# Kernel tuning notes

Measured on AMD Instinct MI355X. Metric: run time of the kernel, lower is better.

The kernel has to match this reference:

```python
import jax, jax.numpy as jnp
import numpy as np

B, L, D = 8, 4096, 768


def setup_inputs() -> dict:
    key = jax.random.key(0)
    k1, = jax.random.split(key, 1)
    x = jax.random.normal(k1, (B, L, D), dtype=jnp.float32)
    alpha = jnp.ones((L, 1), dtype=jnp.float32)  # nn.Parameter(torch.ones(l_dim, 1))
    return {"x": x, "alpha": alpha}


def reference(x, alpha):
    # Original: y = (x @ x^T).mean(-1, keepdim=True) / D
    # Algebraically identical (mean over j of sum_d x_i,d x_j,d = x_i . mean_j x_j):
    d = x.shape[-1]
    l = x.shape[1]
    mean_x = jnp.mean(x, axis=1)                       # [B, D]
    y = jnp.einsum('bld,bd->bl', x, mean_x)[..., None] / d  # [B, L, 1]
    # Original: y = (y @ y^T).mean(-1, keepdim=True) / L
    # (y y^T)_ij = y_i * y_j; mean over j = y_i * mean(y)
    y = y * jnp.mean(y, axis=1, keepdims=True) / l     # [B, L, 1]
    # y * x + alpha  (alpha broadcast over batch and D); dropout p=0 -> identity
    return alpha + y * x
```

## Files before the change

### kernel.cpp

```cpp
#include <hip/hip_runtime.h>

constexpr int Bn = 8;
constexpr int Ln = 4096;
constexpr int Dn = 768;
constexpr int NCH = 128;
constexpr int RPC = Ln / NCH;

typedef float f4 __attribute__((ext_vector_type(4)));

__global__ void k_colsum_part(const float* __restrict__ x, f4* __restrict__ part) {
    int b = blockIdx.x >> 7;
    int c = blockIdx.x & (NCH - 1);
    int t = threadIdx.x;
    const f4* xb = (const f4*)(x + ((size_t)b * Ln + (size_t)c * RPC) * Dn);
    f4 s = {0.f, 0.f, 0.f, 0.f};
    #pragma unroll 4
    for (int l = 0; l < RPC; ++l) {
        s += xb[(size_t)l * (Dn / 4) + t];
    }
    part[(size_t)blockIdx.x * (Dn / 4) + t] = s;
}

__global__ void k_scale(const float* __restrict__ part, float* __restrict__ m) {
    int b = blockIdx.x;
    int t = threadIdx.x;
    const float* pb = part + (size_t)b * NCH * Dn;
    float s0 = 0.f, s1 = 0.f, s2 = 0.f;
    for (int c = 0; c < NCH; ++c) {
        const float* row = pb + (size_t)c * Dn;
        s0 += row[t];
        s1 += row[t + 256];
        s2 += row[t + 512];
    }
    float ssq = s0 * s0 + s1 * s1 + s2 * s2;
    #pragma unroll
    for (int off = 1; off < 64; off <<= 1) ssq += __shfl_xor(ssq, off);
    __shared__ float wsum[4];
    int wave = t >> 6, lane = t & 63;
    if (lane == 0) wsum[wave] = ssq;
    __syncthreads();
    float ss = wsum[0] + wsum[1] + wsum[2] + wsum[3];

    const float f1 = 1.0f / ((float)Ln * (float)Dn);
    float scale = ss * f1 * f1 / ((float)Ln * (float)Ln);
    m[b * Dn + t]       = s0 * scale;
    m[b * Dn + t + 256] = s1 * scale;
    m[b * Dn + t + 512] = s2 * scale;
}

__global__ void k_fused(const float* __restrict__ x, const float* __restrict__ m,
                        const float* __restrict__ alpha, float* __restrict__ out) {
    int wave = threadIdx.x >> 6;
    int lane = threadIdx.x & 63;
    int row  = blockIdx.x * 4 + wave;
    int b    = row >> 12;
    int l    = row & (Ln - 1);

    const f4* xr = (const f4*)(x + (size_t)row * Dn);
    const f4* mr = (const f4*)(m + (size_t)b * Dn);

    f4 x0 = xr[lane], x1 = xr[lane + 64], x2 = xr[lane + 128];
    f4 m0 = mr[lane], m1 = mr[lane + 64], m2 = mr[lane + 128];

    f4 p = x0 * m0 + x1 * m1 + x2 * m2;
    float acc = p.x + p.y + p.z + p.w;
    #pragma unroll
    for (int off = 1; off < 64; off <<= 1) acc += __shfl_xor(acc, off);

    float a = alpha[l];
    f4* orow = (f4*)(out + (size_t)row * Dn);
    f4 o0 = a + acc * x0;
    f4 o1 = a + acc * x1;
    f4 o2 = a + acc * x2;
    __builtin_nontemporal_store(o0, &orow[lane]);
    __builtin_nontemporal_store(o1, &orow[lane + 64]);
    __builtin_nontemporal_store(o2, &orow[lane + 128]);
}

extern "C" void kernel_launch(void* const* d_in, const int* in_sizes, int n_in,
                              void* d_out, int out_size, void* d_ws, size_t ws_size,
                              hipStream_t stream) {
    const float* x     = (const float*)d_in[0];
    const float* alpha = (const float*)d_in[1];
    float* out = (float*)d_out;

    float* part = (float*)d_ws;
    float* m    = part + (size_t)Bn * NCH * Dn;

    k_colsum_part<<<Bn * NCH, 192, 0, stream>>>(x, (f4*)part);
    k_scale<<<Bn, 256, 0, stream>>>(part, m);
    k_fused<<<(Bn * Ln) / 4, 256, 0, stream>>>(x, m, alpha, out);
}
```

Measured before the change: 198.8 us.

## Fuse partial column-sum reduction into the main kernel, dropping the scale kernel

Removes the single-pass k_scale kernel. Each wave of the fused kernel now re-reduces all per-chunk partial sums for its batch and computes the global scale itself. The goal is to save a launch and the serial tail of an 8-block reduction kernel, at the cost of massive redundant reads of the partial buffer, which is mostly served from cache. The colsum loop unroll also rises from 4 to 8.

```diff
diff --git a/kernel.cpp b/kernel.cpp
--- a/kernel.cpp
+++ b/kernel.cpp
@@ -14,53 +14,42 @@
     int t = threadIdx.x;
     const f4* xb = (const f4*)(x + ((size_t)b * Ln + (size_t)c * RPC) * Dn);
     f4 s = {0.f, 0.f, 0.f, 0.f};
-    #pragma unroll 4
+    #pragma unroll 8
     for (int l = 0; l < RPC; ++l) {
         s += xb[(size_t)l * (Dn / 4) + t];
     }
     part[(size_t)blockIdx.x * (Dn / 4) + t] = s;
 }
 
-__global__ void k_scale(const float* __restrict__ part, float* __restrict__ m) {
-    int b = blockIdx.x;
-    int t = threadIdx.x;
-    const float* pb = part + (size_t)b * NCH * Dn;
-    float s0 = 0.f, s1 = 0.f, s2 = 0.f;
-    for (int c = 0; c < NCH; ++c) {
-        const float* row = pb + (size_t)c * Dn;
-        s0 += row[t];
-        s1 += row[t + 256];
-        s2 += row[t + 512];
-    }
-    float ssq = s0 * s0 + s1 * s1 + s2 * s2;
-    #pragma unroll
-    for (int off = 1; off < 64; off <<= 1) ssq += __shfl_xor(ssq, off);
-    __shared__ float wsum[4];
-    int wave = t >> 6, lane = t & 63;
-    if (lane == 0) wsum[wave] = ssq;
-    __syncthreads();
-    float ss = wsum[0] + wsum[1] + wsum[2] + wsum[3];
-
-    const float f1 = 1.0f / ((float)Ln * (float)Dn);
-    float scale = ss * f1 * f1 / ((float)Ln * (float)Ln);
-    m[b * Dn + t]       = s0 * scale;
-    m[b * Dn + t + 256] = s1 * scale;
-    m[b * Dn + t + 512] = s2 * scale;
-}
-
-__global__ void k_fused(const float* __restrict__ x, const float* __restrict__ m,
-                        const float* __restrict__ alpha, float* __restrict__ out) {
+__global__ void __launch_bounds__(256)
+k_fused(const float* __restrict__ x, const float* __restrict__ part,
+        const float* __restrict__ alpha, float* __restrict__ out) {
     int wave = threadIdx.x >> 6;
     int lane = threadIdx.x & 63;
     int row  = blockIdx.x * 4 + wave;
     int b    = row >> 12;
     int l    = row & (Ln - 1);
 
+    const f4* pb = (const f4*)part + (size_t)b * NCH * (Dn / 4);
+    f4 s0 = {0.f,0.f,0.f,0.f}, s1 = {0.f,0.f,0.f,0.f}, s2 = {0.f,0.f,0.f,0.f};
+    #pragma unroll 8
+    for (int c = 0; c < NCH; ++c) {
+        const f4* pr = pb + (size_t)c * (Dn / 4);
+        s0 += pr[lane];
+        s1 += pr[lane + 64];
+        s2 += pr[lane + 128];
+    }
+    f4 q = s0 * s0 + s1 * s1 + s2 * s2;
+    float ssq = q.x + q.y + q.z + q.w;
+    #pragma unroll
+    for (int off = 1; off < 64; off <<= 1) ssq += __shfl_xor(ssq, off);
+
+    const float f1 = 1.0f / ((float)Ln * (float)Dn);
+    float scale = ssq * f1 * f1 / ((float)Ln * (float)Ln);
+    f4 m0 = s0 * scale, m1 = s1 * scale, m2 = s2 * scale;
+
     const f4* xr = (const f4*)(x + (size_t)row * Dn);
-    const f4* mr = (const f4*)(m + (size_t)b * Dn);
-
     f4 x0 = xr[lane], x1 = xr[lane + 64], x2 = xr[lane + 128];
-    f4 m0 = mr[lane], m1 = mr[lane + 64], m2 = mr[lane + 128];
 
     f4 p = x0 * m0 + x1 * m1 + x2 * m2;
     float acc = p.x + p.y + p.z + p.w;
@@ -85,9 +74,7 @@
     float* out = (float*)d_out;
 
     float* part = (float*)d_ws;
-    float* m    = part + (size_t)Bn * NCH * Dn;
 
     k_colsum_part<<<Bn * NCH, 192, 0, stream>>>(x, (f4*)part);
-    k_scale<<<Bn, 256, 0, stream>>>(part, m);
-    k_fused<<<(Bn * Ln) / 4, 256, 0, stream>>>(x, m, alpha, out);
+    k_fused<<<(Bn * Ln) / 4, 256, 0, stream>>>(x, part, alpha, out);
 }
```

Result: slower. 512.3 us (+157.7%).
